# Optimization experiments

Hardware: AMD Instinct MI355X
Metric: run time of the kernel (lower is better)

Reference implementation:

```python
import jax, jax.numpy as jnp
import numpy as np

N_NODES = 100000
IN_DIM = 128
HIDDEN = 128
OUT_DIM = 16
N_EDGES = 1600000


def setup_inputs() -> dict:
    key = jax.random.key(0)
    ks = jax.random.split(key, 10)
    x = jax.random.normal(ks[0], (N_NODES, IN_DIM), dtype=jnp.float32)
    edge_index = jax.random.randint(ks[1], (2, N_EDGES), 0, N_NODES, dtype=jnp.int64)
    s = 1.0 / np.sqrt(IN_DIM)
    W_ego = jax.random.uniform(ks[2], (IN_DIM, HIDDEN), jnp.float32, -s, s)
    b_ego = jax.random.uniform(ks[3], (HIDDEN,), jnp.float32, -s, s)
    W_h1 = jax.random.uniform(ks[4], (IN_DIM, HIDDEN), jnp.float32, -s, s)
    b_h1 = jax.random.uniform(ks[5], (HIDDEN,), jnp.float32, -s, s)
    W_h2 = jax.random.uniform(ks[6], (IN_DIM, HIDDEN), jnp.float32, -s, s)
    b_h2 = jax.random.uniform(ks[7], (HIDDEN,), jnp.float32, -s, s)
    sc = 1.0 / np.sqrt(HIDDEN * 3)
    W_cls = jax.random.uniform(ks[8], (HIDDEN * 3, OUT_DIM), jnp.float32, -sc, sc)
    b_cls = jax.random.uniform(ks[9], (OUT_DIM,), jnp.float32, -sc, sc)
    return {"x": x, "edge_index": edge_index, "W_ego": W_ego, "b_ego": b_ego,
            "W_h1": W_h1, "b_h1": b_h1, "W_h2": W_h2, "b_h2": b_h2,
            "W_cls": W_cls, "b_cls": b_cls}


def reference(x, edge_index, W_ego, b_ego, W_h1, b_h1, W_h2, b_h2, W_cls, b_cls):
    n = x.shape[0]
    row, col = edge_index[0], edge_index[1]
    # degree of source nodes, clamped to >= 1 (as in PyG degree + clamp)
    deg = jax.ops.segment_sum(jnp.ones_like(row, dtype=x.dtype), row, num_segments=n)
    deg_inv = 1.0 / jnp.maximum(deg, 1.0)  # [n]

    def spmm(v):
        # (adj @ v)[i] = sum_{(i,j) in edges} v[j]
        return jax.ops.segment_sum(v[col], row, num_segments=n)

    # ego branch (dropout is identity at inference)
    h_ego = jax.nn.relu(x @ W_ego + b_ego)
    # 1-hop: SpMM + degree norm + linear + relu
    h1 = jax.nn.relu((spmm(x) * deg_inv[:, None]) @ W_h1 + b_h1)
    # 2-hop: SpMM twice + deg^-2 norm + linear + relu
    h2 = jax.nn.relu((spmm(spmm(x)) * (deg_inv ** 2)[:, None]) @ W_h2 + b_h2)

    h = jnp.concatenate([h_ego, h1, h2], axis=1)  # [n, 3*hidden]
    return h @ W_cls + b_cls
```

## Files before the change

kernel.cpp:

```cpp
#include <hip/hip_runtime.h>

#define N_NODES 100000
#define N_EDGES 1600000
#define DIM     128
#define OUTD    16

typedef unsigned int  uint;
typedef unsigned short ushort;
typedef __attribute__((ext_vector_type(8))) short short8;
typedef __attribute__((ext_vector_type(4))) float f32x4;
typedef __attribute__((ext_vector_type(4))) int   i32x4;
typedef __attribute__((ext_vector_type(4))) uint  u32x4;

__device__ __forceinline__ ushort f2bf(float f) {
    uint u = __float_as_uint(f);
    u = u + 0x7fffu + ((u >> 16) & 1u);
    return (ushort)(u >> 16);
}
__device__ __forceinline__ float bflo(uint v) { return __uint_as_float(v << 16); }
__device__ __forceinline__ float bfhi(uint v) { return __uint_as_float(v & 0xffff0000u); }

#define RPB    512
#define NBUCK  196
#define NBLK   500
#define CHUNK4 800
#define BCAP   10240

__global__ __launch_bounds__(256) void k_hist(const int* __restrict__ row,
                                              int* __restrict__ hist) {
    __shared__ int h[NBUCK];
    for (int i = threadIdx.x; i < NBUCK; i += 256) h[i] = 0;
    __syncthreads();
    const i32x4* row4 = (const i32x4*)row;
    int base = blockIdx.x * CHUNK4;
    for (int i = threadIdx.x; i < CHUNK4; i += 256) {
        i32x4 r = __builtin_nontemporal_load(row4 + base + i);
        atomicAdd(&h[r.x >> 9], 1);
        atomicAdd(&h[r.y >> 9], 1);
        atomicAdd(&h[r.z >> 9], 1);
        atomicAdd(&h[r.w >> 9], 1);
    }
    __syncthreads();
    for (int i = threadIdx.x; i < NBUCK; i += 256)
        hist[blockIdx.x * NBUCK + i] = h[i];
}

__global__ void k_scanh(int* __restrict__ hist, int* __restrict__ bucket_base,
                        int* __restrict__ offsets) {
    __shared__ int tot[256];
    int b = threadIdx.x;
    int s = 0;
    if (b < NBUCK) {
#pragma unroll 8
        for (int k = 0; k < NBLK; ++k) {
            int v = hist[k * NBUCK + b];
            hist[k * NBUCK + b] = s;
            s += v;
        }
    }
    tot[b] = (b < NBUCK) ? s : 0;
    __syncthreads();
    for (int off = 1; off < 256; off <<= 1) {
        int a = (b >= off) ? tot[b - off] : 0;
        __syncthreads();
        tot[b] += a;
        __syncthreads();
    }
    int base = tot[b] - s;
    if (b < NBUCK) {
        bucket_base[b] = base;
#pragma unroll 8
        for (int k = 0; k < NBLK; ++k) hist[k * NBUCK + b] += base;
    }
    if (b == NBUCK - 1) {
        bucket_base[NBUCK] = base + s;
        offsets[N_NODES]   = base + s;
    }
}

__global__ __launch_bounds__(256) void k_place(const int* __restrict__ row,
                                               const int* __restrict__ col,
                                               const int* __restrict__ start,
                                               uint* __restrict__ packed) {
    __shared__ int cur[NBUCK];
    for (int i = threadIdx.x; i < NBUCK; i += 256)
        cur[i] = start[blockIdx.x * NBUCK + i];
    __syncthreads();
    const i32x4* row4 = (const i32x4*)row;
    const i32x4* col4 = (const i32x4*)col;
    int base = blockIdx.x * CHUNK4;
    for (int i = threadIdx.x; i < CHUNK4; i += 256) {
        i32x4 r = __builtin_nontemporal_load(row4 + base + i);
        i32x4 c = __builtin_nontemporal_load(col4 + base + i);
        int p;
        p = atomicAdd(&cur[r.x >> 9], 1); packed[p] = ((uint)(r.x & 511) << 17) | (uint)c.x;
        p = atomicAdd(&cur[r.y >> 9], 1); packed[p] = ((uint)(r.y & 511) << 17) | (uint)c.y;
        p = atomicAdd(&cur[r.z >> 9], 1); packed[p] = ((uint)(r.z & 511) << 17) | (uint)c.z;
        p = atomicAdd(&cur[r.w >> 9], 1); packed[p] = ((uint)(r.w & 511) << 17) | (uint)c.w;
    }
}

__global__ __launch_bounds__(256) void k_build(const uint* __restrict__ packed,
                                               const int* __restrict__ bucket_base,
                                               int* __restrict__ deg,
                                               int* __restrict__ offsets,
                                               int* __restrict__ csr_col) {
    __shared__ uint stage[BCAP];
    __shared__ int hist[RPB];
    __shared__ int loff[RPB];
    __shared__ int psum[256];
    int t = threadIdx.x;
    int b = blockIdx.x;
    int base = bucket_base[b];
    int n    = bucket_base[b + 1] - base;
    int lo   = b * RPB;
    bool lds_ok = (n <= BCAP);

    for (int i = t; i < RPB; i += 256) hist[i] = 0;
    __syncthreads();
    if (lds_ok) {
        for (int i = t; i < n; i += 256) {
            uint pk = packed[base + i];
            stage[i] = pk;
            atomicAdd(&hist[pk >> 17], 1);
        }
    } else {
        for (int i = t; i < n; i += 256) atomicAdd(&hist[packed[base + i] >> 17], 1);
    }
    __syncthreads();

    int a0 = hist[2 * t], a1 = hist[2 * t + 1];
    psum[t] = a0 + a1;
    __syncthreads();
    for (int off = 1; off < 256; off <<= 1) {
        int a = (t >= off) ? psum[t - off] : 0;
        __syncthreads();
        psum[t] += a;
        __syncthreads();
    }
    int excl = psum[t] - (a0 + a1);
    loff[2 * t]     = excl;
    loff[2 * t + 1] = excl + a0;
    __syncthreads();

    for (int i = t; i < RPB; i += 256) {
        int node = lo + i;
        if (node < N_NODES) {
            deg[node]     = hist[i];
            offsets[node] = base + loff[i];
        }
    }
    __syncthreads();

    if (lds_ok) {
        for (int i = t; i < n; i += 256) {
            uint pk = stage[i];
            int p = atomicAdd(&loff[pk >> 17], 1);
            csr_col[base + p] = (int)(pk & 0x1FFFFu);
        }
    } else {
        for (int i = t; i < n; i += 256) {
            uint pk = packed[base + i];
            int p = atomicAdd(&loff[pk >> 17], 1);
            csr_col[base + p] = (int)(pk & 0x1FFFFu);
        }
    }
}

__global__ __launch_bounds__(256) void k_convert(
        const float4* __restrict__ x4,
        const float* __restrict__ We, const float* __restrict__ W1,
        const float* __restrict__ W2, const float* __restrict__ Wc,
        ushort* __restrict__ xb, ushort* __restrict__ Wt, ushort* __restrict__ Wct) {
    int tid = blockIdx.x * blockDim.x + threadIdx.x;
    int stride = gridDim.x * blockDim.x;
    for (int i = tid; i < N_NODES * DIM / 4; i += stride) {
        float4 v = x4[i];
        ushort4 r;
        r.x = f2bf(v.x); r.y = f2bf(v.y); r.z = f2bf(v.z); r.w = f2bf(v.w);
        *(ushort4*)(xb + (size_t)i * 4) = r;
    }
    for (int i = tid; i < 3 * DIM * DIM; i += stride) {
        int b = i >> 14, r2 = i & (DIM * DIM - 1);
        int k = r2 >> 7, n = r2 & 127;
        const float* W = (b == 0) ? We : (b == 1) ? W1 : W2;
        Wt[b * DIM * DIM + n * DIM + k] = f2bf(W[r2]);
    }
    for (int i = tid; i < 384 * OUTD; i += stride) {
        int k = i >> 4, o = i & 15;
        Wct[o * 384 + k] = f2bf(Wc[i]);
    }
}

__global__ __launch_bounds__(256) void k_spmm(const ushort* __restrict__ in,
                                              ushort* __restrict__ outp,
                                              const int* __restrict__ offsets,
                                              const int* __restrict__ csr_col) {
    int wid = threadIdx.x >> 6, lane = threadIdx.x & 63;
    int sub = lane >> 4, sl = lane & 15;
    int node = blockIdx.x * 4 + wid;
    int start = __builtin_amdgcn_readfirstlane(offsets[node]);
    int end   = __builtin_amdgcn_readfirstlane(offsets[node + 1]);
    float f0 = 0.f, f1 = 0.f, f2 = 0.f, f3 = 0.f;
    float f4 = 0.f, f5 = 0.f, f6 = 0.f, f7 = 0.f;
    int j = start;
    for (; j + 8 <= end; j += 8) {
        int cA = csr_col[j + sub];
        int cB = csr_col[j + 4 + sub];
        u32x4 a = *(const u32x4*)(in + ((size_t)cA << 7) + sl * 8);
        u32x4 b = *(const u32x4*)(in + ((size_t)cB << 7) + sl * 8);
        f0 += bflo(a.x) + bflo(b.x); f1 += bfhi(a.x) + bfhi(b.x);
        f2 += bflo(a.y) + bflo(b.y); f3 += bfhi(a.y) + bfhi(b.y);
        f4 += bflo(a.z) + bflo(b.z); f5 += bfhi(a.z) + bfhi(b.z);
        f6 += bflo(a.w) + bflo(b.w); f7 += bfhi(a.w) + bfhi(b.w);
    }
    for (; j < end; j += 4) {
        if (j + sub < end) {
            int c = csr_col[j + sub];
            u32x4 a = *(const u32x4*)(in + ((size_t)c << 7) + sl * 8);
            f0 += bflo(a.x); f1 += bfhi(a.x);
            f2 += bflo(a.y); f3 += bfhi(a.y);
            f4 += bflo(a.z); f5 += bfhi(a.z);
            f6 += bflo(a.w); f7 += bfhi(a.w);
        }
    }
    f0 += __shfl_xor(f0, 16, 64); f0 += __shfl_xor(f0, 32, 64);
    f1 += __shfl_xor(f1, 16, 64); f1 += __shfl_xor(f1, 32, 64);
    f2 += __shfl_xor(f2, 16, 64); f2 += __shfl_xor(f2, 32, 64);
    f3 += __shfl_xor(f3, 16, 64); f3 += __shfl_xor(f3, 32, 64);
    f4 += __shfl_xor(f4, 16, 64); f4 += __shfl_xor(f4, 32, 64);
    f5 += __shfl_xor(f5, 16, 64); f5 += __shfl_xor(f5, 32, 64);
    f6 += __shfl_xor(f6, 16, 64); f6 += __shfl_xor(f6, 32, 64);
    f7 += __shfl_xor(f7, 16, 64); f7 += __shfl_xor(f7, 32, 64);
    if (sub == 0) {
        uint o0 = (uint)f2bf(f0) | ((uint)f2bf(f1) << 16);
        uint o1 = (uint)f2bf(f2) | ((uint)f2bf(f3) << 16);
        uint o2 = (uint)f2bf(f4) | ((uint)f2bf(f5) << 16);
        uint o3 = (uint)f2bf(f6) | ((uint)f2bf(f7) << 16);
        u32x4 ov = {o0, o1, o2, o3};
        __builtin_nontemporal_store(ov, (u32x4*)(outp + ((size_t)node << 7) + sl * 8));
    }
}

#define XSS (DIM + 8)

__global__ __launch_bounds__(256) void k_fused(
        const ushort* __restrict__ xb, const ushort* __restrict__ y1r,
        const ushort* __restrict__ y2r, const int* __restrict__ deg,
        const ushort* __restrict__ Wt, const ushort* __restrict__ Wct,
        const float* __restrict__ b_ego, const float* __restrict__ b_h1,
        const float* __restrict__ b_h2, const float* __restrict__ b_cls,
        float* __restrict__ out) {
    __shared__ __align__(16) ushort Xs[32 * XSS];
    __shared__ __align__(16) ushort Hs[32 * XSS];

    int t = threadIdx.x;
    int lane = t & 63, w = t >> 6;
    int q = lane >> 4, l = lane & 15;
    int node0 = blockIdx.x * 32;

    float dvv[2][4];
#pragma unroll
    for (int mt = 0; mt < 2; ++mt) {
        int4 dg = *(const int4*)(deg + node0 + mt * 16 + q * 4);
        dvv[mt][0] = 1.f / (float)max(dg.x, 1);
        dvv[mt][1] = 1.f / (float)max(dg.y, 1);
        dvv[mt][2] = 1.f / (float)max(dg.z, 1);
        dvv[mt][3] = 1.f / (float)max(dg.w, 1);
    }

    f32x4 cout0 = {0.f, 0.f, 0.f, 0.f}, cout1 = {0.f, 0.f, 0.f, 0.f};

    for (int br = 0; br < 3; ++br) {
        const ushort* src = (br == 0) ? xb : (br == 1) ? y1r : y2r;
        const ushort* Wtb = Wt + br * DIM * DIM;
        const float* bias = (br == 0) ? b_ego : (br == 1) ? b_h1 : b_h2;

        __syncthreads();
        {
            int row = t >> 3, col = (t & 7) * 16;
            const ushort* sp = src + ((size_t)(node0 + row) << 7) + col;
            uint4 u0 = *(const uint4*)sp;
            uint4 u1 = *(const uint4*)(sp + 8);
            *(uint4*)(Xs + row * XSS + col) = u0;
            *(uint4*)(Xs + row * XSS + col + 8) = u1;
        }
        __syncthreads();

        short8 afr[2][4];
#pragma unroll
        for (int mt = 0; mt < 2; ++mt)
#pragma unroll
            for (int ks = 0; ks < 4; ++ks)
                afr[mt][ks] = *(const short8*)(Xs + (mt * 16 + l) * XSS + ks * 32 + q * 8);
        short8 bfr[2][4];
#pragma unroll
        for (int nt = 0; nt < 2; ++nt)
#pragma unroll
            for (int ks = 0; ks < 4; ++ks)
                bfr[nt][ks] = *(const short8*)(Wtb + (size_t)(w * 32 + nt * 16 + l) * DIM + ks * 32 + q * 8);

        f32x4 hc[2][2];
        hc[0][0] = hc[0][1] = hc[1][0] = hc[1][1] = (f32x4){0.f, 0.f, 0.f, 0.f};
#pragma unroll
        for (int ks = 0; ks < 4; ++ks)
#pragma unroll
            for (int mt = 0; mt < 2; ++mt)
#pragma unroll
                for (int nt = 0; nt < 2; ++nt)
                    hc[mt][nt] = __builtin_amdgcn_mfma_f32_16x16x32_bf16(
                        afr[mt][ks], bfr[nt][ks], hc[mt][nt], 0, 0, 0);

#pragma unroll
        for (int nt = 0; nt < 2; ++nt) {
            float bv = bias[w * 32 + nt * 16 + l];
#pragma unroll
            for (int mt = 0; mt < 2; ++mt)
#pragma unroll
                for (int r = 0; r < 4; ++r) {
                    float s = (br == 0) ? 1.f
                            : (br == 1) ? dvv[mt][r]
                                        : dvv[mt][r] * dvv[mt][r];
                    float v = hc[mt][nt][r] * s + bv;
                    v = v > 0.f ? v : 0.f;
                    Hs[(mt * 16 + q * 4 + r) * XSS + w * 32 + nt * 16 + l] = f2bf(v);
                }
        }
        __syncthreads();

        short8 ha0 = *(const short8*)(Hs + l * XSS + w * 32 + q * 8);
        short8 ha1 = *(const short8*)(Hs + (16 + l) * XSS + w * 32 + q * 8);
        short8 wc  = *(const short8*)(Wct + (size_t)l * 384 + br * DIM + w * 32 + q * 8);
        cout0 = __builtin_amdgcn_mfma_f32_16x16x32_bf16(ha0, wc, cout0, 0, 0, 0);
        cout1 = __builtin_amdgcn_mfma_f32_16x16x32_bf16(ha1, wc, cout1, 0, 0, 0);
    }

    float* red = (float*)Xs;
#pragma unroll
    for (int r = 0; r < 4; ++r) {
        red[w * 512 + (q * 4 + r) * 16 + l]      = cout0[r];
        red[w * 512 + (16 + q * 4 + r) * 16 + l] = cout1[r];
    }
    __syncthreads();
#pragma unroll
    for (int p = t; p < 512; p += 256) {
        float s = red[p] + red[512 + p] + red[1024 + p] + red[1536 + p];
        out[(size_t)node0 * OUTD + p] = s + b_cls[p & 15];
    }
}

static inline size_t align256(size_t v) { return (v + 255) & ~(size_t)255; }

extern "C" void kernel_launch(void* const* d_in, const int* in_sizes, int n_in,
                              void* d_out, int out_size, void* d_ws, size_t ws_size,
                              hipStream_t stream) {
    const float* x      = (const float*)d_in[0];
    const int*   ei     = (const int*)d_in[1];
    const float* W_ego  = (const float*)d_in[2];
    const float* b_ego  = (const float*)d_in[3];
    const float* W_h1   = (const float*)d_in[4];
    const float* b_h1   = (const float*)d_in[5];
    const float* W_h2   = (const float*)d_in[6];
    const float* b_h2   = (const float*)d_in[7];
    const float* W_cls  = (const float*)d_in[8];
    const float* b_cls  = (const float*)d_in[9];
    float* out = (float*)d_out;

    const int* row = ei;
    const int* col = ei + N_EDGES;

    char* p = (char*)d_ws;
    int* deg       = (int*)p;    p += align256((size_t)N_NODES * 4);
    int* offsets   = (int*)p;    p += align256((size_t)(N_NODES + 1) * 4);
    int* hist      = (int*)p;    p += align256((size_t)NBLK * NBUCK * 4);
    int* bbase     = (int*)p;    p += align256((size_t)(NBUCK + 1) * 4);
    uint* packed   = (uint*)p;   p += align256((size_t)N_EDGES * 4);
    int* csr_col   = (int*)p;    p += align256((size_t)N_EDGES * 4);
    ushort* xb     = (ushort*)p; p += align256((size_t)N_NODES * DIM * 2);
    ushort* y1r    = (ushort*)p; p += align256((size_t)N_NODES * DIM * 2);
    ushort* y2r    = (ushort*)p; p += align256((size_t)N_NODES * DIM * 2);
    ushort* Wt     = (ushort*)p; p += align256((size_t)3 * DIM * DIM * 2);
    ushort* Wct    = (ushort*)p; p += align256((size_t)384 * OUTD * 2);

    k_hist<<<NBLK, 256, 0, stream>>>(row, hist);
    k_convert<<<2048, 256, 0, stream>>>((const float4*)x, W_ego, W_h1, W_h2, W_cls,
                                        xb, Wt, Wct);
    k_scanh<<<1, 256, 0, stream>>>(hist, bbase, offsets);
    k_place<<<NBLK, 256, 0, stream>>>(row, col, hist, packed);
    k_build<<<NBUCK, 256, 0, stream>>>(packed, bbase, deg, offsets, csr_col);

    k_spmm<<<N_NODES / 4, 256, 0, stream>>>(xb,  y1r, offsets, csr_col);
    k_spmm<<<N_NODES / 4, 256, 0, stream>>>(y1r, y2r, offsets, csr_col);

    k_fused<<<N_NODES / 32, 256, 0, stream>>>(xb, y1r, y2r, deg, Wt, Wct,
                                              b_ego, b_h1, b_h2, b_cls, out);
}
```

Baseline: 381.1 us.

## Parallelize histogram scan across buckets with per-bucket blocks and a separate totals scan

Replaces the single-block serial scan over 500 histogram rows with one block per bucket that does a parallel prefix scan over the per-block counts. A tiny second kernel then scans the bucket totals. The bucket base is now added in the placement kernel instead of being written back into the histogram. This removes a long serial dependent-load loop running on one CU, at the cost of one extra kernel launch and a small extra buffer.

```diff
diff --git a/kernel.cpp b/kernel.cpp
--- a/kernel.cpp
+++ b/kernel.cpp
@@ -45,46 +45,60 @@
         hist[blockIdx.x * NBUCK + i] = h[i];
 }
 
-__global__ void k_scanh(int* __restrict__ hist, int* __restrict__ bucket_base,
+__global__ __launch_bounds__(256) void k_scanb(int* __restrict__ hist,
+                                               int* __restrict__ btot) {
+    __shared__ int psum[256];
+    int b = blockIdx.x, t = threadIdx.x;
+    int v0 = 0, v1 = 0;
+    if (t < NBLK / 2) {
+        v0 = hist[(2 * t) * NBUCK + b];
+        v1 = hist[(2 * t + 1) * NBUCK + b];
+    }
+    int s = v0 + v1;
+    psum[t] = s;
+    __syncthreads();
+    for (int off = 1; off < 256; off <<= 1) {
+        int a = (t >= off) ? psum[t - off] : 0;
+        __syncthreads();
+        psum[t] += a;
+        __syncthreads();
+    }
+    int excl = psum[t] - s;
+    if (t < NBLK / 2) {
+        hist[(2 * t) * NBUCK + b]     = excl;
+        hist[(2 * t + 1) * NBUCK + b] = excl + v0;
+    }
+    if (t == 255) btot[b] = psum[255];
+}
+
+__global__ void k_scant(const int* __restrict__ btot, int* __restrict__ bbase,
                         int* __restrict__ offsets) {
-    __shared__ int tot[256];
-    int b = threadIdx.x;
-    int s = 0;
-    if (b < NBUCK) {
-#pragma unroll 8
-        for (int k = 0; k < NBLK; ++k) {
-            int v = hist[k * NBUCK + b];
-            hist[k * NBUCK + b] = s;
-            s += v;
-        }
-    }
-    tot[b] = (b < NBUCK) ? s : 0;
+    __shared__ int s[256];
+    int t = threadIdx.x;
+    int v = (t < NBUCK) ? btot[t] : 0;
+    s[t] = v;
     __syncthreads();
     for (int off = 1; off < 256; off <<= 1) {
-        int a = (b >= off) ? tot[b - off] : 0;
-        __syncthreads();
-        tot[b] += a;
-        __syncthreads();
-    }
-    int base = tot[b] - s;
-    if (b < NBUCK) {
-        bucket_base[b] = base;
-#pragma unroll 8
-        for (int k = 0; k < NBLK; ++k) hist[k * NBUCK + b] += base;
-    }
-    if (b == NBUCK - 1) {
-        bucket_base[NBUCK] = base + s;
-        offsets[N_NODES]   = base + s;
+        int a = (t >= off) ? s[t - off] : 0;
+        __syncthreads();
+        s[t] += a;
+        __syncthreads();
+    }
+    if (t < NBUCK) bbase[t] = s[t] - v;
+    if (t == NBUCK - 1) {
+        bbase[NBUCK]     = s[t];
+        offsets[N_NODES] = s[t];
     }
 }
 
 __global__ __launch_bounds__(256) void k_place(const int* __restrict__ row,
                                                const int* __restrict__ col,
                                                const int* __restrict__ start,
+                                               const int* __restrict__ bbase,
                                                uint* __restrict__ packed) {
     __shared__ int cur[NBUCK];
     for (int i = threadIdx.x; i < NBUCK; i += 256)
-        cur[i] = start[blockIdx.x * NBUCK + i];
+        cur[i] = start[blockIdx.x * NBUCK + i] + bbase[i];
     __syncthreads();
     const i32x4* row4 = (const i32x4*)row;
     const i32x4* col4 = (const i32x4*)col;
@@ -374,6 +388,7 @@
     int* offsets   = (int*)p;    p += align256((size_t)(N_NODES + 1) * 4);
     int* hist      = (int*)p;    p += align256((size_t)NBLK * NBUCK * 4);
     int* bbase     = (int*)p;    p += align256((size_t)(NBUCK + 1) * 4);
+    int* btot      = (int*)p;    p += align256((size_t)NBUCK * 4);
     uint* packed   = (uint*)p;   p += align256((size_t)N_EDGES * 4);
     int* csr_col   = (int*)p;    p += align256((size_t)N_EDGES * 4);
     ushort* xb     = (ushort*)p; p += align256((size_t)N_NODES * DIM * 2);
@@ -385,8 +400,9 @@
     k_hist<<<NBLK, 256, 0, stream>>>(row, hist);
     k_convert<<<2048, 256, 0, stream>>>((const float4*)x, W_ego, W_h1, W_h2, W_cls,
                                         xb, Wt, Wct);
-    k_scanh<<<1, 256, 0, stream>>>(hist, bbase, offsets);
-    k_place<<<NBLK, 256, 0, stream>>>(row, col, hist, packed);
+    k_scanb<<<NBUCK, 256, 0, stream>>>(hist, btot);
+    k_scant<<<1, 256, 0, stream>>>(btot, bbase, offsets);
+    k_place<<<NBLK, 256, 0, stream>>>(row, col, hist, bbase, packed);
     k_build<<<NBUCK, 256, 0, stream>>>(packed, bbase, deg, offsets, csr_col);
 
     k_spmm<<<N_NODES / 4, 256, 0, stream>>>(xb,  y1r, offsets, csr_col);
```

After: 317.6 us. 16.7% less time.
